# Optimization experiments

Measured on AMD Instinct MI355X. Metric: run time of the kernel, lower is better.

The kernel has to match this reference:

```python
import jax, jax.numpy as jnp
import numpy as np
import math

B, L, D_MODEL = 8, 1024, 512
D_INNER = 1024          # expand*d_model
D2 = D_INNER // 2       # per-branch channels
DT_RANK = 32            # ceil(d_model/16)
D_STATE = 16
K = 4                   # d_conv
HIDDEN = 4 * D_MODEL


def setup_inputs() -> dict:
    key = jax.random.key(0)
    ks = jax.random.split(key, 12)
    rn = lambda k, s, sc: jax.random.normal(k, s, jnp.float32) * sc
    x = rn(ks[0], (B, L, D_MODEL), 1.0)
    in_proj_w = rn(ks[1], (D_INNER, D_MODEL), D_MODEL ** -0.5)
    conv_x_w = rn(ks[2], (D2, 1, K), 0.2)
    conv_z_w = rn(ks[3], (D2, 1, K), 0.2)
    x_proj_w = rn(ks[4], (DT_RANK + 2 * D_STATE, D2), D2 ** -0.5)
    dt_proj_w = rn(ks[5], (D2, DT_RANK), DT_RANK ** -0.5)
    dt = jnp.exp(jax.random.uniform(ks[6], (D2,)) * (math.log(0.1) - math.log(0.001)) + math.log(0.001))
    dt_proj_b = dt + jnp.log(-jnp.expm1(-dt))  # inverse softplus
    A_log = jnp.log(jnp.tile(jnp.arange(1, D_STATE + 1, dtype=jnp.float32)[None, :], (D2, 1)))
    ssm_D = jnp.ones((D2,), jnp.float32)
    out_proj_w = rn(ks[7], (D_MODEL, D_INNER), D_INNER ** -0.5)
    fc1_w = rn(ks[8], (HIDDEN, D_MODEL), D_MODEL ** -0.5)
    fc2_w = rn(ks[9], (D_MODEL, HIDDEN), HIDDEN ** -0.5)
    return dict(x=x,
                ln1_w=jnp.ones((D_MODEL,)), ln1_b=jnp.zeros((D_MODEL,)),
                in_proj_w=in_proj_w, conv_x_w=conv_x_w, conv_z_w=conv_z_w,
                x_proj_w=x_proj_w, dt_proj_w=dt_proj_w, dt_proj_b=dt_proj_b,
                A_log=A_log, ssm_D=ssm_D, out_proj_w=out_proj_w,
                ln2_w=jnp.ones((D_MODEL,)), ln2_b=jnp.zeros((D_MODEL,)),
                fc1_w=fc1_w, fc1_b=jnp.zeros((HIDDEN,)),
                fc2_w=fc2_w, fc2_b=jnp.zeros((D_MODEL,)))


def _layernorm(x, w, b, eps=1e-5):
    m = jnp.mean(x, -1, keepdims=True)
    v = jnp.mean((x - m) ** 2, -1, keepdims=True)
    return (x - m) * jax.lax.rsqrt(v + eps) * w + b


def _dwconv1d_same(x, w):
    # x: (b, c, l); w: (c, 1, K). torch 'same' for even K pads (left=1, right=2)
    return jax.lax.conv_general_dilated(
        x, w, window_strides=(1,), padding=[(1, 2)],
        dimension_numbers=('NCH', 'OIH', 'NCH'), feature_group_count=x.shape[1])


def _selective_scan(u, delta, A, Bc, Cc, Dp):
    # u, delta: (b, d, l); A: (d, n); Bc, Cc: (b, n, l); Dp: (d,)
    dA = jnp.exp(delta[..., None] * A[None, :, None, :])            # (b,d,l,n)
    Bt = jnp.moveaxis(Bc, 2, 1)                                     # (b,l,n)
    dBu = (delta * u)[..., None] * Bt[:, None, :, :]                # (b,d,l,n)
    dA_l = jnp.moveaxis(dA, 2, 0)                                   # (l,b,d,n)
    dBu_l = jnp.moveaxis(dBu, 2, 0)

    def step(h, t):
        dAt, dBut = t
        h = dAt * h + dBut
        return h, h

    h0 = jnp.zeros((u.shape[0], u.shape[1], A.shape[1]), u.dtype)
    _, hs = jax.lax.scan(step, h0, (dA_l, dBu_l))                   # hs: (l,b,d,n)
    Ct = jnp.moveaxis(Cc, 2, 0)                                     # (l,b,n)
    y = jnp.einsum('lbdn,lbn->bdl', hs, Ct)
    return y + Dp[None, :, None] * u


def _mixer(xn, in_proj_w, conv_x_w, conv_z_w, x_proj_w, dt_proj_w, dt_proj_b, A_log, ssm_D, out_proj_w):
    # xn: (b, l, d_model)
    xz = jnp.einsum('bld,ed->bel', xn, in_proj_w)                   # (b, d_inner, l)
    xh, zh = jnp.split(xz, 2, axis=1)                               # (b, d2, l) each
    xh = jax.nn.silu(_dwconv1d_same(xh, conv_x_w))
    zh = jax.nn.silu(_dwconv1d_same(zh, conv_z_w))
    x_dbl = jnp.einsum('bdl,rd->brl', xh, x_proj_w)                 # (b, R+2n, l)
    dt, Bc, Cc = jnp.split(x_dbl, [DT_RANK, DT_RANK + D_STATE], axis=1)
    dt = jnp.einsum('brl,dr->bdl', dt, dt_proj_w)
    delta = jax.nn.softplus(dt + dt_proj_b[None, :, None])          # delta_bias + delta_softplus
    A = -jnp.exp(A_log)
    y = _selective_scan(xh, delta, A, Bc, Cc, ssm_D)                # (b, d2, l)
    out = jnp.concatenate([y, zh], axis=1)                          # (b, d_inner, l)
    return jnp.einsum('bdl,ed->ble', out, out_proj_w)               # (b, l, d_model)


def reference(x, ln1_w, ln1_b, in_proj_w, conv_x_w, conv_z_w, x_proj_w, dt_proj_w, dt_proj_b,
              A_log, ssm_D, out_proj_w, ln2_w, ln2_b, fc1_w, fc1_b, fc2_w, fc2_b):
    h = x + _mixer(_layernorm(x, ln1_w, ln1_b), in_proj_w, conv_x_w, conv_z_w,
                   x_proj_w, dt_proj_w, dt_proj_b, A_log, ssm_D, out_proj_w)
    h2 = _layernorm(h, ln2_w, ln2_b)
    mlp = jax.nn.gelu(h2 @ fc1_w.T + fc1_b, approximate=False) @ fc2_w.T + fc2_b
    return h + mlp
```

## Files before the change

### kernel.cpp

```cpp
#include <hip/hip_runtime.h>
#include <stdint.h>


#define MROWS 8192
#define LSEQ 1024
#define DMODEL 512
#define DINNER 1024
#define D2 512
#define NSTATE 16
#define HIDDEN 2048
#define NCHUNK 32
#define LCHUNK 32

typedef unsigned short us;
typedef short short8 __attribute__((ext_vector_type(8)));
typedef float floatx4 __attribute__((ext_vector_type(4)));

__device__ __forceinline__ us f2bf(float f) {
    unsigned int u = __float_as_uint(f);
    u = (u + 0x7fffu + ((u >> 16) & 1u)) >> 16;
    return (us)u;
}
__device__ __forceinline__ float bf2f(us u) {
    return __uint_as_float(((unsigned int)u) << 16);
}

__device__ __forceinline__ void g2lds16(const void* g, void* l) {
    typedef __attribute__((address_space(1))) void GV;
    typedef __attribute__((address_space(3))) void LV;
    GV* gp = (GV*)(uintptr_t)g;
    LV* lp = (LV*)(uint32_t)(uintptr_t)l;
    __builtin_amdgcn_global_load_lds(gp, lp, 16, 0, 0);
}

__device__ __forceinline__ void pack_slot(const float* __restrict__ w,
                                          us* __restrict__ dst, int K, int sig)
{
    int lane = sig & 63;
    int KS = K >> 5;
    int ks = (sig >> 6) % KS;
    int g = sig / (KS << 6);
    const float* src = w + (size_t)(g * 16 + (lane & 15)) * K
                         + ks * 32 + (lane >> 4) * 8;
    short8 o;
    #pragma unroll
    for (int e = 0; e < 8; e++) o[e] = (short)f2bf(src[e]);
    *(short8*)(dst + (size_t)sig * 8) = o;
}

__global__ __launch_bounds__(256) void cvt_pack6(
    const float* __restrict__ w0, const float* __restrict__ w1,
    const float* __restrict__ w2, const float* __restrict__ w3,
    const float* __restrict__ w4, const float* __restrict__ w5,
    us* __restrict__ o0, us* __restrict__ o1, us* __restrict__ o2,
    us* __restrict__ o3, us* __restrict__ o4, us* __restrict__ o5)
{
    int bx = blockIdx.x, t = threadIdx.x;
    if (bx < 256)        pack_slot(w0, o0, 512,  bx * 256 + t);
    else if (bx < 272)   pack_slot(w1, o1, 512,  (bx - 256) * 256 + t);
    else if (bx < 280)   pack_slot(w2, o2, 32,   (bx - 272) * 256 + t);
    else if (bx < 536)   pack_slot(w3, o3, 1024, (bx - 280) * 256 + t);
    else if (bx < 1048)  pack_slot(w4, o4, 512,  (bx - 536) * 256 + t);
    else                 pack_slot(w5, o5, 2048, (bx - 1048) * 256 + t);
}

__global__ __launch_bounds__(256) void ln_pack(
    const float* __restrict__ x, const float* __restrict__ w,
    const float* __restrict__ b, us* __restrict__ outp)
{
    int g = blockIdx.x, t = threadIdx.x;
    __shared__ float T[16][516];
    __shared__ float mu[16], rs[16];
    const float* src = x + (size_t)g * 16 * DMODEL;
    #pragma unroll
    for (int p = 0; p < 8; p++) {
        int idx4 = p * 256 + t;
        int row = idx4 >> 7, c = (idx4 & 127) << 2;
        float4 v = *(const float4*)(src + (size_t)row * DMODEL + c);
        *(float4*)&T[row][c] = v;
    }
    __syncthreads();
    int r = t >> 4, i = t & 15;
    float s = 0.f, ss = 0.f;
    #pragma unroll
    for (int c = 0; c < 32; c++) {
        float v = T[r][c * 16 + i];
        s += v; ss += v * v;
    }
    #pragma unroll
    for (int off = 8; off > 0; off >>= 1) {
        s += __shfl_down(s, off, 16);
        ss += __shfl_down(ss, off, 16);
    }
    if (i == 0) {
        float m = s * (1.f / DMODEL);
        mu[r] = m;
        rs[r] = rsqrtf(ss * (1.f / DMODEL) - m * m + 1e-5f);
    }
    __syncthreads();
    #pragma unroll
    for (int s0 = 0; s0 < 4; s0++) {
        int sig = t * 4 + s0;
        int lane = sig & 63, ks = sig >> 6;
        int lr = lane & 15, lq = lane >> 4;
        int k0 = ks * 32 + lq * 8;
        float m = mu[lr], r2 = rs[lr];
        short8 o;
        #pragma unroll
        for (int e = 0; e < 8; e++)
            o[e] = (short)f2bf((T[lr][k0 + e] - m) * r2 * w[k0 + e] + b[k0 + e]);
        *(short8*)(outp + (size_t)g * 8192 + sig * 8) = o;
    }
}

#define MO_ROWBF16 0
#define MO_F32_PACK 1
#define MO_SOFTPLUS 2
#define MO_RES 3
#define MO_GELU_PACK 4
#define MO_BIAS_RES 5

template <int MODE, int BN>
__global__ __launch_bounds__(256) void gemm_pk2(
    const us* __restrict__ Ap, const us* __restrict__ Bp, int K,
    int Nout, int ldc,
    float* __restrict__ outF, us* __restrict__ outB, us* __restrict__ outP,
    const float* __restrict__ bias, const float* __restrict__ res)
{
    constexpr int NBg = BN / 16;
    constexpr int NJ = BN / 32;
    constexpr int TS = 8 + 2 * NBg;
    constexpr int PS = TS / 4;
    constexpr int STG = TS * 1024;
    constexpr int TTS = 32 * (BN + 4) * 4;
    constexpr int SM = STG > TTS ? STG : TTS;
    __shared__ __align__(16) char smraw[SM];
    us* sA = (us*)smraw;
    us* sB = sA + 8 * 512;
    float (*TT)[BN + 4] = (float (*)[BN + 4])smraw;

    int t = threadIdx.x;
    int lane = t & 63, w = t >> 6;
    int lr = lane & 15, lq = lane >> 4;
    int m0 = blockIdx.x * 64, n0 = blockIdx.y * BN;
    int gA0 = blockIdx.x * 4;
    int gB0 = blockIdx.y * NBg;
    int KS32 = K >> 5;

    floatx4 acc[2][NJ];
    #pragma unroll
    for (int i = 0; i < 2; i++)
        #pragma unroll
        for (int j = 0; j < NJ; j++) acc[i][j] = (floatx4){0.f, 0.f, 0.f, 0.f};

    for (int k64 = 0; k64 * 64 < K; k64++) {
        #pragma unroll
        for (int s = 0; s < PS; s++) {
            int slot = w * PS + s;
            if (slot < 8) {
                int g = slot >> 1, kl = slot & 1;
                g2lds16(Ap + ((size_t)(gA0 + g) * KS32 + k64 * 2 + kl) * 512
                           + lane * 8,
                        sA + slot * 512);
            } else {
                int sl = slot - 8;
                int j = sl >> 1, kl = sl & 1;
                g2lds16(Bp + ((size_t)(gB0 + j) * KS32 + k64 * 2 + kl) * 512
                           + lane * 8,
                        sB + sl * 512);
            }
        }
        __syncthreads();
        #pragma unroll
        for (int kl = 0; kl < 2; kl++) {
            short8 af[2], bfv[NJ];
            #pragma unroll
            for (int i = 0; i < 2; i++)
                af[i] = *(const short8*)(sA + (((w & 1) * 2 + i) * 2 + kl) * 512
                                         + lane * 8);
            #pragma unroll
            for (int j = 0; j < NJ; j++)
                bfv[j] = *(const short8*)(sB + (((w >> 1) * NJ + j) * 2 + kl) * 512
                                          + lane * 8);
            #pragma unroll
            for (int i = 0; i < 2; i++)
                #pragma unroll
                for (int j = 0; j < NJ; j++)
                    acc[i][j] = __builtin_amdgcn_mfma_f32_16x16x32_bf16(
                        af[i], bfv[j], acc[i][j], 0, 0, 0);
        }
        __syncthreads();
    }

    #pragma unroll
    for (int h = 0; h < 2; h++) {
        if ((w & 1) == h) {
            #pragma unroll
            for (int i = 0; i < 2; i++)
                #pragma unroll
                for (int j = 0; j < NJ; j++)
                    #pragma unroll
                    for (int r = 0; r < 4; r++)
                        TT[i * 16 + lq * 4 + r]
                          [(w >> 1) * (BN / 2) + j * 16 + lr] = acc[i][j][r];
        }
        __syncthreads();

        if (MODE == MO_ROWBF16) {
            constexpr int passes = 32 * BN / 8 / 256;
            #pragma unroll
            for (int p = 0; p < passes; p++) {
                int idx = p * 256 + t;
                int row = idx / (BN / 8);
                int c = (idx % (BN / 8)) * 8;
                short8 o8;
                #pragma unroll
                for (int e = 0; e < 8; e++) o8[e] = (short)f2bf(TT[row][c + e]);
                *(short8*)(outB + (size_t)(m0 + h * 32 + row) * ldc + n0 + c) = o8;
            }
        }
        if (MODE == MO_F32_PACK || MODE == MO_RES || MODE == MO_BIAS_RES) {
            constexpr int passes = 32 * BN / 4 / 256;
            #pragma unroll
            for (int p = 0; p < passes; p++) {
                int idx = p * 256 + t;
                int row = idx / (BN / 4);
                int c = (idx % (BN / 4)) * 4;
                float4 v = *(float4*)&TT[row][c];
                int col = n0 + c;
                size_t o = (size_t)(m0 + h * 32 + row) * ldc + col;
                float4 ov;
                if (MODE == MO_RES) {
                    float4 rv = *(const float4*)(res + o);
                    ov.x = v.x + rv.x; ov.y = v.y + rv.y;
                    ov.z = v.z + rv.z; ov.w = v.w + rv.w;
                } else if (MODE == MO_BIAS_RES) {
                    float4 rv = *(const float4*)(res + o);
                    float4 bv = *(const float4*)(bias + col);
                    ov.x = v.x + bv.x + rv.x; ov.y = v.y + bv.y + rv.y;
                    ov.z = v.z + bv.z + rv.z; ov.w = v.w + bv.w + rv.w;
                } else {
                    ov = v;
                }
                *(float4*)(outF + o) = ov;
            }
        }
        if (MODE == MO_F32_PACK || MODE == MO_GELU_PACK) {
            constexpr int passes = 4 * BN / 256;
            #pragma unroll
            for (int p = 0; p < passes; p++) {
                int sig = p * 256 + t;
                int gi = sig / (2 * BN);
                int rem = sig % (2 * BN);
                int ksl = rem >> 6;
                int ln2 = rem & 63;
                int lr2 = ln2 & 15, lq2 = ln2 >> 4;
                short8 o8;
                #pragma unroll
                for (int e = 0; e < 8; e++) {
                    float vv = TT[gi * 16 + lr2][ksl * 32 + lq2 * 8 + e];
                    if (MODE == MO_GELU_PACK) {
                        float tb = vv + bias[n0 + ksl * 32 + lq2 * 8 + e];
                        vv = 0.5f * tb * (1.f + erff(tb * 0.70710678118f));
                    }
                    o8[e] = (short)f2bf(vv);
                }
                *(short8*)(outP + ((size_t)((m0 >> 4) + h * 2 + gi) * Nout
                           + n0 + ksl * 32) * 16 + ln2 * 8) = o8;
            }
        }
        __syncthreads();
    }
}

template <int MODE, int BN>
__global__ __launch_bounds__(256) void gemm_pk(
    const us* __restrict__ Ap, int KA,
    const us* __restrict__ Bp, int KB, int Kloop,
    int Nout, int ldc,
    float* __restrict__ outF, us* __restrict__ outB, us* __restrict__ outP,
    const float* __restrict__ bias, const float* __restrict__ res)
{
    constexpr int NBg = BN / 16;
    constexpr int NJ = BN / 32;
    constexpr int TS = 4 + NBg;
    constexpr int PS = TS / 4;
    constexpr int SMSZ = 64 * (BN + 4) * 4;
    __shared__ __align__(16) char smraw[SMSZ];
    us* sA = (us*)smraw;
    us* sB = sA + 2048;
    float (*TT)[BN + 4] = (float (*)[BN + 4])smraw;

    int t = threadIdx.x;
    int lane = t & 63, w = t >> 6;
    int lr = lane & 15, lq = lane >> 4;
    int m0 = blockIdx.x * 64, n0 = blockIdx.y * BN;
    int gA0 = blockIdx.x * 4;
    int gB0 = n0 >> 4;

    floatx4 acc[2][NJ];
    #pragma unroll
    for (int i = 0; i < 2; i++)
        #pragma unroll
        for (int j = 0; j < NJ; j++) acc[i][j] = (floatx4){0.f, 0.f, 0.f, 0.f};

    for (int ks = 0; ks * 32 < Kloop; ks++) {
        #pragma unroll
        for (int s = 0; s < PS; s++) {
            int slot = w * PS + s;
            if (slot < 4)
                g2lds16(Ap + ((size_t)(gA0 + slot) * KA + ks * 32) * 16 + lane * 8,
                        sA + slot * 512);
            else
                g2lds16(Bp + ((size_t)(gB0 + slot - 4) * KB + ks * 32) * 16 + lane * 8,
                        sB + (slot - 4) * 512);
        }
        __syncthreads();
        short8 af[2], bfv[NJ];
        #pragma unroll
        for (int i = 0; i < 2; i++)
            af[i] = *(const short8*)(sA + ((w & 1) * 2 + i) * 512 + lane * 8);
        #pragma unroll
        for (int j = 0; j < NJ; j++)
            bfv[j] = *(const short8*)(sB + ((w >> 1) * NJ + j) * 512 + lane * 8);
        #pragma unroll
        for (int i = 0; i < 2; i++)
            #pragma unroll
            for (int j = 0; j < NJ; j++)
                acc[i][j] = __builtin_amdgcn_mfma_f32_16x16x32_bf16(
                    af[i], bfv[j], acc[i][j], 0, 0, 0);
        __syncthreads();
    }

    #pragma unroll
    for (int i = 0; i < 2; i++)
        #pragma unroll
        for (int j = 0; j < NJ; j++)
            #pragma unroll
            for (int r = 0; r < 4; r++)
                TT[(w & 1) * 32 + i * 16 + lq * 4 + r]
                  [(w >> 1) * (BN / 2) + j * 16 + lr] = acc[i][j][r];
    __syncthreads();

    if (MODE == MO_SOFTPLUS) {
        constexpr int passes = 64 * BN / 4 / 256;
        #pragma unroll
        for (int p = 0; p < passes; p++) {
            int idx = p * 256 + t;
            int row = idx / (BN / 4);
            int c = (idx % (BN / 4)) * 4;
            float4 v = *(float4*)&TT[row][c];
            int col = n0 + c;
            size_t o = (size_t)(m0 + row) * ldc + col;
            float vv[4] = {v.x, v.y, v.z, v.w};
            float oo[4];
            #pragma unroll
            for (int e = 0; e < 4; e++) {
                float tb = vv[e] + bias[col + e];
                oo[e] = (tb > 20.f) ? tb : log1pf(__expf(tb));
            }
            float4 ov = {oo[0], oo[1], oo[2], oo[3]};
            *(float4*)(outF + o) = ov;
        }
    }
}

__global__ __launch_bounds__(256) void conv_pk(
    const us* __restrict__ xz, const float* __restrict__ cwx,
    const float* __restrict__ cwz, float* __restrict__ xh_f,
    us* __restrict__ xh_p, us* __restrict__ outbuf_p)
{
    int bx = blockIdx.x, t = threadIdx.x;
    int b = bx >> 6, g = bx & 63;
    size_t rowbase = (size_t)b * LSEQ;
    #pragma unroll
    for (int s = 0; s < 4; s++) {
        int sig = t * 4 + s;
        int ks = sig >> 6, lane = sig & 63;
        int lr = lane & 15, lq = lane >> 4;
        int l = g * 16 + lr;
        int d0 = ks * 32 + lq * 8;
        float ax[8] = {0, 0, 0, 0, 0, 0, 0, 0};
        #pragma unroll
        for (int kk = 0; kk < 4; kk++) {
            int ls = l + kk - 1;
            if (ls >= 0 && ls < LSEQ) {
                const us* src = xz + (rowbase + ls) * DINNER + d0;
                #pragma unroll
                for (int e = 0; e < 8; e++)
                    ax[e] += cwx[(d0 + e) * 4 + kk] * bf2f(src[e]);
            }
        }
        short8 o8;
        float vo[8];
        #pragma unroll
        for (int e = 0; e < 8; e++) {
            float v = ax[e];
            v = v / (1.f + __expf(-v));
            vo[e] = v;
            o8[e] = (short)f2bf(v);
        }
        *(short8*)(xh_p + (size_t)bx * 8192 + sig * 8) = o8;
        float* fo = xh_f + (rowbase + l) * D2 + d0;
        float4 f0 = {vo[0], vo[1], vo[2], vo[3]};
        float4 f1 = {vo[4], vo[5], vo[6], vo[7]};
        *(float4*)fo = f0;
        *(float4*)(fo + 4) = f1;
    }
    #pragma unroll
    for (int s = 0; s < 4; s++) {
        int sig = t * 4 + s;
        int ks = sig >> 6, lane = sig & 63;
        int lr = lane & 15, lq = lane >> 4;
        int l = g * 16 + lr;
        int d0 = ks * 32 + lq * 8;
        float az[8] = {0, 0, 0, 0, 0, 0, 0, 0};
        #pragma unroll
        for (int kk = 0; kk < 4; kk++) {
            int ls = l + kk - 1;
            if (ls >= 0 && ls < LSEQ) {
                const us* src = xz + (rowbase + ls) * DINNER + 512 + d0;
                #pragma unroll
                for (int e = 0; e < 8; e++)
                    az[e] += cwz[(d0 + e) * 4 + kk] * bf2f(src[e]);
            }
        }
        short8 o8;
        #pragma unroll
        for (int e = 0; e < 8; e++) {
            float v = az[e];
            v = v / (1.f + __expf(-v));
            o8[e] = (short)f2bf(v);
        }
        *(short8*)(outbuf_p + (size_t)bx * 16384 + 8192 + sig * 8) = o8;
    }
}

__global__ __launch_bounds__(256) void scan_phase1(
    const float* __restrict__ delta, const float* __restrict__ u,
    const float* __restrict__ xdbl, const float* __restrict__ A_log,
    float* __restrict__ S, float* __restrict__ P)
{
    int bx = blockIdx.x;
    int b = bx >> 6, rem = bx & 63, c = rem >> 1, half = rem & 1;
    int d = half * 256 + threadIdx.x;
    float A2[NSTATE], h[NSTATE];
    #pragma unroll
    for (int n = 0; n < NSTATE; n++) {
        A2[n] = -__expf(A_log[d * NSTATE + n]) * 1.44269504f;
        h[n] = 0.f;
    }
    float sdt = 0.f;
    int l0 = c * LCHUNK;
    for (int l = l0; l < l0 + LCHUNK; ++l) {
        size_t idx = (size_t)(b * LSEQ + l);
        float dv = delta[idx * D2 + d];
        float uv = u[idx * D2 + d];
        float du = dv * uv;
        const float4* Bp = (const float4*)(xdbl + idx * 64 + 32);
        float4 B0 = Bp[0], B1 = Bp[1], B2 = Bp[2], B3 = Bp[3];
        float Bn[16] = {B0.x, B0.y, B0.z, B0.w, B1.x, B1.y, B1.z, B1.w,
                        B2.x, B2.y, B2.z, B2.w, B3.x, B3.y, B3.z, B3.w};
        sdt += dv;
        #pragma unroll
        for (int n = 0; n < NSTATE; n++)
            h[n] = exp2f(dv * A2[n]) * h[n] + du * Bn[n];
    }
    size_t o = ((size_t)(b * D2 + d)) * (NCHUNK * NSTATE) + c * NSTATE;
    #pragma unroll
    for (int n = 0; n < NSTATE; n++) {
        S[o + n] = h[n];
        P[o + n] = exp2f(sdt * A2[n]);
    }
}

__global__ __launch_bounds__(256) void scan_phase2(
    const float* __restrict__ S, const float* __restrict__ P,
    float* __restrict__ hin)
{
    int gid = blockIdx.x * 256 + threadIdx.x;
    int n = gid & 15;
    size_t base = ((size_t)(gid >> 4)) * (NCHUNK * NSTATE) + n;
    float h = 0.f;
    for (int c = 0; c < NCHUNK; c++) {
        size_t o = base + c * NSTATE;
        hin[o] = h;
        h = P[o] * h + S[o];
    }
}

__global__ __launch_bounds__(256) void scan_phase3(
    const float* __restrict__ delta, const float* __restrict__ u,
    const float* __restrict__ xdbl, const float* __restrict__ hin,
    const float* __restrict__ A_log, const float* __restrict__ Dvec,
    us* __restrict__ outbuf_p)
{
    int bx = blockIdx.x;
    int b = bx >> 6, rem = bx & 63, c = rem >> 1, half = rem & 1;
    int t = threadIdx.x;
    int d = half * 256 + t;
    __shared__ us yl[LCHUNK][264];
    float A2[NSTATE], h[NSTATE];
    size_t hb = ((size_t)(b * D2 + d)) * (NCHUNK * NSTATE) + c * NSTATE;
    #pragma unroll
    for (int n = 0; n < NSTATE; n++) {
        A2[n] = -__expf(A_log[d * NSTATE + n]) * 1.44269504f;
        h[n] = hin[hb + n];
    }
    float Dd = Dvec[d];
    int l0 = c * LCHUNK;
    for (int l = l0; l < l0 + LCHUNK; ++l) {
        size_t idx = (size_t)(b * LSEQ + l);
        float dv = delta[idx * D2 + d];
        float uv = u[idx * D2 + d];
        float du = dv * uv;
        const float4* Bp = (const float4*)(xdbl + idx * 64 + 32);
        const float4* Cp = (const float4*)(xdbl + idx * 64 + 48);
        float4 B0 = Bp[0], B1 = Bp[1], B2 = Bp[2], B3 = Bp[3];
        float4 C0 = Cp[0], C1 = Cp[1], C2 = Cp[2], C3 = Cp[3];
        float Bn[16] = {B0.x, B0.y, B0.z, B0.w, B1.x, B1.y, B1.z, B1.w,
                        B2.x, B2.y, B2.z, B2.w, B3.x, B3.y, B3.z, B3.w};
        float Cn[16] = {C0.x, C0.y, C0.z, C0.w, C1.x, C1.y, C1.z, C1.w,
                        C2.x, C2.y, C2.z, C2.w, C3.x, C3.y, C3.z, C3.w};
        float y = Dd * uv;
        #pragma unroll
        for (int n = 0; n < NSTATE; n++) {
            h[n] = exp2f(dv * A2[n]) * h[n] + du * Bn[n];
            y += h[n] * Cn[n];
        }
        yl[l - l0][t] = f2bf(y);
    }
    __syncthreads();
    int g0 = (b * LSEQ + l0) >> 4;
    #pragma unroll
    for (int s = 0; s < 4; s++) {
        int sig = t * 4 + s;
        int gi = sig >> 9;
        int rem2 = sig & 511;
        int ksl = rem2 >> 6;
        int lane = rem2 & 63;
        int lr = lane & 15, lq = lane >> 4;
        uint4 v = *(uint4*)&yl[gi * 16 + lr][ksl * 32 + lq * 8];
        *(uint4*)(outbuf_p + ((size_t)(g0 + gi) * 1024 + (half * 8 + ksl) * 32) * 16
                  + lane * 8) = v;
    }
}

extern "C" void kernel_launch(void* const* d_in, const int* in_sizes, int n_in,
                              void* d_out, int out_size, void* d_ws, size_t ws_size,
                              hipStream_t stream)
{
    const float* x         = (const float*)d_in[0];
    const float* ln1_w     = (const float*)d_in[1];
    const float* ln1_b     = (const float*)d_in[2];
    const float* in_proj_w = (const float*)d_in[3];
    const float* conv_x_w  = (const float*)d_in[4];
    const float* conv_z_w  = (const float*)d_in[5];
    const float* x_proj_w  = (const float*)d_in[6];
    const float* dt_proj_w = (const float*)d_in[7];
    const float* dt_proj_b = (const float*)d_in[8];
    const float* A_log     = (const float*)d_in[9];
    const float* ssm_D     = (const float*)d_in[10];
    const float* out_proj_w= (const float*)d_in[11];
    const float* ln2_w     = (const float*)d_in[12];
    const float* ln2_b     = (const float*)d_in[13];
    const float* fc1_w     = (const float*)d_in[14];
    const float* fc1_b     = (const float*)d_in[15];
    const float* fc2_w     = (const float*)d_in[16];
    const float* fc2_b     = (const float*)d_in[17];
    float* out = (float*)d_out;

    char* p = (char*)d_ws;
    us* wp_in  = (us*)(p);
    us* wp_x   = (us*)(p + 1048576);
    us* wp_dt  = (us*)(p + 1114112);
    us* wp_out = (us*)(p + 1146880);
    us* wp_f1  = (us*)(p + 2195456);
    us* wp_f2  = (us*)(p + 4292608);
    us*    xn_p    = (us*)(p + 6389760);
    us*    xz      = (us*)(p + 14778368);
    us*    xh_p    = (us*)(p + 31555584);
    float* xh_f    = (float*)(p + 39944192);
    us*    outbuf_p= (us*)(p + 56721408);
    float* xdbl_f  = (float*)(p + 73498624);
    us*    xdbl_p  = (us*)(p + 75595776);
    float* delta_f = (float*)(p + 76644352);
    float* h_f     = (float*)(p + 106004480);
    us*    h2_p    = xn_p;
    us*    mlp1_p  = xz;
    float* scanS = (float*)(p + 14778368);
    float* scanP = (float*)(p + 14778368 + 8388608);
    float* hin   = (float*)(p + 6389760);

    cvt_pack6<<<1560, 256, 0, stream>>>(in_proj_w, x_proj_w, dt_proj_w,
        out_proj_w, fc1_w, fc2_w, wp_in, wp_x, wp_dt, wp_out, wp_f1, wp_f2);

    ln_pack<<<512, 256, 0, stream>>>(x, ln1_w, ln1_b, xn_p);

    gemm_pk2<MO_ROWBF16, 128><<<dim3(128, 8), 256, 0, stream>>>(
        xn_p, wp_in, 512, 0, DINNER, nullptr, xz, nullptr, nullptr, nullptr);

    conv_pk<<<512, 256, 0, stream>>>(xz, conv_x_w, conv_z_w, xh_f, xh_p, outbuf_p);

    gemm_pk2<MO_F32_PACK, 64><<<dim3(128, 1), 256, 0, stream>>>(
        xh_p, wp_x, 512, 64, 64, xdbl_f, nullptr, xdbl_p, nullptr, nullptr);

    gemm_pk<MO_SOFTPLUS, 64><<<dim3(128, 8), 256, 0, stream>>>(
        xdbl_p, 64, wp_dt, 32, 32, 0, D2,
        delta_f, nullptr, nullptr, dt_proj_b, nullptr);

    scan_phase1<<<512, 256, 0, stream>>>(delta_f, xh_f, xdbl_f, A_log, scanS, scanP);
    scan_phase2<<<256, 256, 0, stream>>>(scanS, scanP, hin);
    scan_phase3<<<512, 256, 0, stream>>>(delta_f, xh_f, xdbl_f, hin, A_log,
        ssm_D, outbuf_p);

    gemm_pk2<MO_RES, 128><<<dim3(128, 4), 256, 0, stream>>>(
        outbuf_p, wp_out, 1024, 0, DMODEL, h_f, nullptr, nullptr, nullptr, x);

    ln_pack<<<512, 256, 0, stream>>>(h_f, ln2_w, ln2_b, h2_p);

    gemm_pk2<MO_GELU_PACK, 128><<<dim3(128, 16), 256, 0, stream>>>(
        h2_p, wp_f1, 512, HIDDEN, 0, nullptr, nullptr, mlp1_p, fc1_b, nullptr);

    gemm_pk2<MO_BIAS_RES, 128><<<dim3(128, 4), 256, 0, stream>>>(
        mlp1_p, wp_f2, 2048, 0, DMODEL, out, nullptr, nullptr, fc2_b, h_f);
}
```

Before: 328.7 us.

## Add 128x128-tile GEMM for in_proj and fc1, use tanh-form GELU

Adds a gemm_big kernel that computes 128x128 output tiles per block, with each wave holding a 4x4 set of MFMA accumulators. This raises arithmetic intensity and halves the grid for the in_proj and fc1 GEMMs. The exact erf GELU is replaced by a tanh-approximation written with an exponential, which is cheaper to evaluate but differs numerically from the reference's approximate=False GELU. The new kernel loads a K-slice and then syncs, with no double buffering, so load latency may be less well hidden, and the larger tile may lower occupancy.

Result: no change. 332.1 us (+1.0%).

```diff
diff --git a/kernel.cpp b/kernel.cpp
--- a/kernel.cpp
+++ b/kernel.cpp
@@ -24,6 +24,11 @@
 __device__ __forceinline__ float bf2f(us u) {
     return __uint_as_float(((unsigned int)u) << 16);
 }
+__device__ __forceinline__ float gelu_fast(float x) {
+    float u = 1.59576912f * (x + 0.044715f * x * x * x);
+    float e = __expf(u);
+    return x * e / (e + 1.f) ;
+}
 
 __device__ __forceinline__ void g2lds16(const void* g, void* l) {
     typedef __attribute__((address_space(1))) void GV;
@@ -119,6 +124,124 @@
 #define MO_RES 3
 #define MO_GELU_PACK 4
 #define MO_BIAS_RES 5
+
+template <int MODE>
+__global__ __launch_bounds__(256) void gemm_big(
+    const us* __restrict__ Ap, const us* __restrict__ Bp, int K,
+    int Nout, int ldc,
+    float* __restrict__ outF, us* __restrict__ outB, us* __restrict__ outP,
+    const float* __restrict__ bias, const float* __restrict__ res)
+{
+    __shared__ __align__(16) char smraw[32768];
+    us* sA = (us*)smraw;
+    us* sB = sA + 16 * 512;
+    float (*TT)[132] = (float (*)[132])smraw;
+
+    int t = threadIdx.x;
+    int lane = t & 63, w = t >> 6;
+    int lr = lane & 15, lq = lane >> 4;
+    int m0 = blockIdx.x * 128, n0 = blockIdx.y * 128;
+    int gA0 = blockIdx.x * 8;
+    int gB0 = blockIdx.y * 8;
+    int KS32 = K >> 5;
+    int wmh = w & 1;
+    int wnh = w >> 1;
+
+    floatx4 acc[4][4];
+    #pragma unroll
+    for (int i = 0; i < 4; i++)
+        #pragma unroll
+        for (int j = 0; j < 4; j++) acc[i][j] = (floatx4){0.f, 0.f, 0.f, 0.f};
+
+    for (int k64 = 0; k64 * 64 < K; k64++) {
+        #pragma unroll
+        for (int s = 0; s < 8; s++) {
+            int slot = w * 8 + s;
+            if (slot < 16) {
+                int g = slot >> 1, kl = slot & 1;
+                g2lds16(Ap + ((size_t)(gA0 + g) * KS32 + k64 * 2 + kl) * 512
+                           + lane * 8,
+                        sA + slot * 512);
+            } else {
+                int sl = slot - 16;
+                int j = sl >> 1, kl = sl & 1;
+                g2lds16(Bp + ((size_t)(gB0 + j) * KS32 + k64 * 2 + kl) * 512
+                           + lane * 8,
+                        sB + sl * 512);
+            }
+        }
+        __syncthreads();
+        #pragma unroll
+        for (int kl = 0; kl < 2; kl++) {
+            short8 af[4], bfv[4];
+            #pragma unroll
+            for (int i = 0; i < 4; i++)
+                af[i] = *(const short8*)(sA + ((wmh * 4 + i) * 2 + kl) * 512
+                                         + lane * 8);
+            #pragma unroll
+            for (int j = 0; j < 4; j++)
+                bfv[j] = *(const short8*)(sB + ((wnh * 4 + j) * 2 + kl) * 512
+                                          + lane * 8);
+            #pragma unroll
+            for (int i = 0; i < 4; i++)
+                #pragma unroll
+                for (int j = 0; j < 4; j++)
+                    acc[i][j] = __builtin_amdgcn_mfma_f32_16x16x32_bf16(
+                        af[i], bfv[j], acc[i][j], 0, 0, 0);
+        }
+        __syncthreads();
+    }
+
+    #pragma unroll
+    for (int h = 0; h < 4; h++) {
+        if (wmh == (h >> 1)) {
+            int i0 = (h & 1) * 2;
+            #pragma unroll
+            for (int ii = 0; ii < 2; ii++)
+                #pragma unroll
+                for (int j = 0; j < 4; j++)
+                    #pragma unroll
+                    for (int r = 0; r < 4; r++)
+                        TT[ii * 16 + lq * 4 + r]
+                          [wnh * 64 + j * 16 + lr] = acc[i0 + ii][j][r];
+        }
+        __syncthreads();
+
+        if (MODE == MO_ROWBF16) {
+            #pragma unroll
+            for (int p = 0; p < 2; p++) {
+                int idx = p * 256 + t;
+                int row = idx >> 4;
+                int c = (idx & 15) * 8;
+                short8 o8;
+                #pragma unroll
+                for (int e = 0; e < 8; e++) o8[e] = (short)f2bf(TT[row][c + e]);
+                *(short8*)(outB + (size_t)(m0 + h * 32 + row) * ldc + n0 + c) = o8;
+            }
+        }
+        if (MODE == MO_GELU_PACK) {
+            #pragma unroll
+            for (int p = 0; p < 2; p++) {
+                int sig = p * 256 + t;
+                int gi = sig >> 8;
+                int rem = sig & 255;
+                int ksl = rem >> 6;
+                int ln2 = rem & 63;
+                int lr2 = ln2 & 15, lq2 = ln2 >> 4;
+                short8 o8;
+                #pragma unroll
+                for (int e = 0; e < 8; e++) {
+                    float tb = TT[gi * 16 + lr2][ksl * 32 + lq2 * 8 + e]
+                               + bias[n0 + ksl * 32 + lq2 * 8 + e];
+                    o8[e] = (short)f2bf(gelu_fast(tb));
+                }
+                *(short8*)(outP + ((size_t)((m0 >> 4) + h * 2 + gi) * Nout
+                           + n0 + ksl * 32) * 16 + ln2 * 8) = o8;
+            }
+        }
+        __syncthreads();
+    }
+}
 
 template <int MODE, int BN>
 __global__ __launch_bounds__(256) void gemm_pk2(
@@ -261,7 +384,7 @@
                     float vv = TT[gi * 16 + lr2][ksl * 32 + lq2 * 8 + e];
                     if (MODE == MO_GELU_PACK) {
                         float tb = vv + bias[n0 + ksl * 32 + lq2 * 8 + e];
-                        vv = 0.5f * tb * (1.f + erff(tb * 0.70710678118f));
+                        vv = gelu_fast(tb);
                     }
                     o8[e] = (short)f2bf(vv);
                 }
@@ -597,7 +720,7 @@
 
     ln_pack<<<512, 256, 0, stream>>>(x, ln1_w, ln1_b, xn_p);
 
-    gemm_pk2<MO_ROWBF16, 128><<<dim3(128, 8), 256, 0, stream>>>(
+    gemm_big<MO_ROWBF16><<<dim3(64, 8), 256, 0, stream>>>(
         xn_p, wp_in, 512, 0, DINNER, nullptr, xz, nullptr, nullptr, nullptr);
 
     conv_pk<<<512, 256, 0, stream>>>(xz, conv_x_w, conv_z_w, xh_f, xh_p, outbuf_p);
@@ -619,7 +742,7 @@
 
     ln_pack<<<512, 256, 0, stream>>>(h_f, ln2_w, ln2_b, h2_p);
 
-    gemm_pk2<MO_GELU_PACK, 128><<<dim3(128, 16), 256, 0, stream>>>(
+    gemm_big<MO_GELU_PACK><<<dim3(64, 16), 256, 0, stream>>>(
         h2_p, wp_f1, 512, HIDDEN, 0, nullptr, nullptr, mlp1_p, fc1_b, nullptr);
 
     gemm_pk2<MO_BIAS_RES, 128><<<dim3(128, 4), 256, 0, stream>>>(
```
